# Optimization experiments

Measured on AMD Instinct MI355X. Metric: run time of the kernel, lower is better.

The kernel has to match this reference:

```python
import jax, jax.numpy as jnp
import numpy as np

D_MODEL = 1024
EXPAND = 4
D_INNER = EXPAND * D_MODEL  # 4096
D_STATE = 16
D_CONV = 4
DT_RANK = (D_MODEL + 15) // 16  # 64
B_SZ, L_SEQ = 2, 2048
EPS = 1e-5


def _quantize(w):
    # round(clamp(w / mean|w|, -1, 1)) -> ternary weights
    s = w / (jnp.mean(jnp.abs(w)) + 1e-8)
    return jnp.round(jnp.clip(s, -1.0, 1.0))


def setup_inputs() -> dict:
    key = jax.random.key(0)
    ks = jax.random.split(key, 16)
    f32 = jnp.float32
    x = jax.random.normal(ks[0], (B_SZ, L_SEQ, D_MODEL), dtype=f32)
    # LayerNorms
    g1 = jnp.ones((D_MODEL,), f32); b1 = jnp.zeros((D_MODEL,), f32)
    g2 = jnp.ones((D_MODEL,), f32); b2 = jnp.zeros((D_MODEL,), f32)
    # SwiGLU MLP (ternary-quantized weights, as in __init__)
    w1 = _quantize(jax.random.normal(ks[1], (EXPAND * D_MODEL, D_MODEL), f32) * 0.02)
    bias1 = jnp.zeros((EXPAND * D_MODEL,), f32)
    w2 = _quantize(jax.random.normal(ks[2], (D_MODEL, EXPAND * D_MODEL), f32) * 0.02)
    bias2 = jnp.zeros((D_MODEL,), f32)
    # Mamba params
    in_proj_w = jax.random.normal(ks[3], (2 * D_INNER, D_MODEL), f32) * 0.02
    conv_w = jax.random.normal(ks[4], (D_INNER, D_CONV), f32) * 0.2
    conv_b = jnp.zeros((D_INNER,), f32)
    x_proj_w = jax.random.normal(ks[5], (DT_RANK + 2 * D_STATE, D_INNER), f32) * 0.02
    dt_proj_w = jax.random.normal(ks[6], (D_INNER, DT_RANK), f32) * (DT_RANK ** -0.5)
    dt_proj_b = jnp.log(jnp.expm1(jnp.clip(
        jnp.exp(jax.random.uniform(ks[7], (D_INNER,), f32) * (np.log(0.1) - np.log(1e-3)) + np.log(1e-3)),
        1e-4, None)))  # standard mamba dt bias init
    A_log = jnp.log(jnp.broadcast_to(jnp.arange(1, D_STATE + 1, dtype=f32), (D_INNER, D_STATE)))
    D = jnp.ones((D_INNER,), f32)
    out_proj_w = jax.random.normal(ks[8], (D_MODEL, D_INNER), f32) * 0.02
    return dict(x=x, g1=g1, b1=b1, g2=g2, b2=b2, w1=w1, bias1=bias1, w2=w2, bias2=bias2,
                in_proj_w=in_proj_w, conv_w=conv_w, conv_b=conv_b, x_proj_w=x_proj_w,
                dt_proj_w=dt_proj_w, dt_proj_b=dt_proj_b, A_log=A_log, D=D,
                out_proj_w=out_proj_w)


def _layernorm(x, g, b):
    mu = jnp.mean(x, -1, keepdims=True)
    var = jnp.mean(jnp.square(x - mu), -1, keepdims=True)
    return (x - mu) * jax.lax.rsqrt(var + EPS) * g + b


def _mamba(xn, in_proj_w, conv_w, conv_b, x_proj_w, dt_proj_w, dt_proj_b, A_log, D, out_proj_w):
    B, L, _ = xn.shape
    xz = jnp.einsum('bld,ed->ble', xn, in_proj_w)  # [B,L,2*d_inner]
    u, z = jnp.split(xz, 2, axis=-1)
    # causal depthwise conv1d, kernel size D_CONV
    up = jnp.pad(u, ((0, 0), (D_CONV - 1, 0), (0, 0)))
    conv = conv_b + sum(up[:, k:k + L, :] * conv_w[:, k] for k in range(D_CONV))
    u = jax.nn.silu(conv)  # [B,L,d_inner]
    x_dbl = jnp.einsum('bld,ed->ble', u, x_proj_w)
    dt_in, Bm, Cm = jnp.split(x_dbl, [DT_RANK, DT_RANK + D_STATE], axis=-1)
    dt = jax.nn.softplus(jnp.einsum('blr,dr->bld', dt_in, dt_proj_w) + dt_proj_b)
    A = -jnp.exp(A_log)  # [d_inner, d_state]

    def step(h, inp):
        dt_t, B_t, C_t, u_t = inp  # [B,d_inner],[B,d_state],[B,d_state],[B,d_inner]
        dA = jnp.exp(dt_t[..., None] * A)              # [B,d_inner,d_state]
        h = dA * h + (dt_t * u_t)[..., None] * B_t[:, None, :]
        y = jnp.einsum('bds,bs->bd', h, C_t)
        return h, y

    h0 = jnp.zeros((B, D_INNER, D_STATE), xn.dtype)
    xs = (dt.swapaxes(0, 1), Bm.swapaxes(0, 1), Cm.swapaxes(0, 1), u.swapaxes(0, 1))
    _, ys = jax.lax.scan(step, h0, xs)
    y = ys.swapaxes(0, 1) + u * D
    y = y * jax.nn.silu(z)
    return jnp.einsum('ble,de->bld', y, out_proj_w)


def reference(x, g1, b1, g2, b2, w1, bias1, w2, bias2, in_proj_w, conv_w, conv_b,
              x_proj_w, dt_proj_w, dt_proj_b, A_log, D, out_proj_w):
    h = _layernorm(x, g1, b1)
    h = jax.nn.silu(jnp.einsum('bld,ed->ble', h, w1) + bias1)
    x = x + jnp.einsum('ble,de->bld', h, w2) + bias2
    x = x + _mamba(_layernorm(x, g2, b2), in_proj_w, conv_w, conv_b, x_proj_w,
                   dt_proj_w, dt_proj_b, A_log, D, out_proj_w)
    return x
```

## Files before the change

### kernel.cpp

```cpp
#include <hip/hip_runtime.h>
#include <cstdint>
#include <cstddef>


namespace {
constexpr int D_MODEL = 1024;
constexpr int D_INNER = 4096;
constexpr int D_STATE = 16;
constexpr int DT_RANK = 64;
constexpr int B_SZ    = 2;
constexpr int L_SEQ   = 2048;
constexpr int M_ROWS  = B_SZ * L_SEQ;
constexpr int LC      = 64;
constexpr int NCHUNK  = L_SEQ / LC;
}

typedef __bf16 bf16x8_t __attribute__((ext_vector_type(8)));
typedef float  f32x4    __attribute__((ext_vector_type(4)));

__device__ __forceinline__ unsigned short f2bf(float f) {
  union { float f; unsigned int u; } v; v.f = f;
  unsigned int r = (v.u + 0x7fffu + ((v.u >> 16) & 1u)) >> 16;
  return (unsigned short)r;
}
__device__ __forceinline__ float bf2f(unsigned short s) {
  union { unsigned int u; float f; } v; v.u = ((unsigned int)s) << 16;
  return v.f;
}

__device__ __forceinline__ float softplus_fast(float v) {
  const float e = __builtin_amdgcn_exp2f(-fabsf(v) * 1.44269504088896f);
  return fmaxf(v, 0.f) + 0.693147180559945f * __builtin_amdgcn_logf(1.f + e);
}

__device__ __forceinline__ void gload16(const void* g, void* l) {
  __builtin_amdgcn_global_load_lds(
      (const __attribute__((address_space(1))) unsigned int*)g,
      (__attribute__((address_space(3))) unsigned int*)l, 16, 0, 0);
}

__global__ __launch_bounds__(256)
void cvt6(const float* __restrict__ s0, unsigned short* __restrict__ d0,
          const float* __restrict__ s1, unsigned short* __restrict__ d1,
          const float* __restrict__ s2, unsigned short* __restrict__ d2,
          const float* __restrict__ s3, unsigned short* __restrict__ d3,
          const float* __restrict__ s4, unsigned short* __restrict__ d4,
          const float* __restrict__ s5, unsigned short* __restrict__ d5) {
  int blk = blockIdx.x;
  const float* s; unsigned short* d;
  if (blk < 4096)                  { s = s0; d = d0; }
  else if ((blk -= 4096) < 4096)   { s = s1; d = d1; }
  else if ((blk -= 4096) < 8192)   { s = s2; d = d2; }
  else if ((blk -= 8192) < 384)    { s = s3; d = d3; }
  else if ((blk -= 384) < 256)     { s = s4; d = d4; }
  else { blk -= 256;                 s = s5; d = d5; }
  const int i = blk * 1024 + threadIdx.x * 4;
  float4 v = *(const float4*)(s + i);
  ushort4 o; o.x = f2bf(v.x); o.y = f2bf(v.y); o.z = f2bf(v.z); o.w = f2bf(v.w);
  *(ushort4*)(d + i) = o;
}

__global__ __launch_bounds__(256) void ln_bf16(const float* __restrict__ x,
                                               const float* __restrict__ g,
                                               const float* __restrict__ b,
                                               unsigned short* __restrict__ out) {
  const int row = blockIdx.x;
  const int tid = threadIdx.x;
  const float4 v = *(const float4*)(x + (size_t)row * D_MODEL + tid * 4);
  float s  = v.x + v.y + v.z + v.w;
  float s2 = v.x*v.x + v.y*v.y + v.z*v.z + v.w*v.w;
#pragma unroll
  for (int o = 32; o >= 1; o >>= 1) { s += __shfl_xor(s, o); s2 += __shfl_xor(s2, o); }
  __shared__ float red[8];
  if ((tid & 63) == 0) { red[(tid >> 6) * 2] = s; red[(tid >> 6) * 2 + 1] = s2; }
  __syncthreads();
  s  = red[0] + red[2] + red[4] + red[6];
  s2 = red[1] + red[3] + red[5] + red[7];
  const float mu  = s * (1.f / D_MODEL);
  const float var = s2 * (1.f / D_MODEL) - mu * mu;
  const float rstd = rsqrtf(var + 1e-5f);
  const float4 gv = *(const float4*)(g + tid * 4);
  const float4 bv = *(const float4*)(b + tid * 4);
  ushort4 o;
  o.x = f2bf((v.x - mu) * rstd * gv.x + bv.x);
  o.y = f2bf((v.y - mu) * rstd * gv.y + bv.y);
  o.z = f2bf((v.z - mu) * rstd * gv.z + bv.z);
  o.w = f2bf((v.w - mu) * rstd * gv.w + bv.w);
  *(ushort4*)(out + (size_t)row * D_MODEL + tid * 4) = o;
}

__global__ __launch_bounds__(256)
void combine_ln(const float* __restrict__ part, const float* __restrict__ bias,
                const float* __restrict__ res, const float* __restrict__ g,
                const float* __restrict__ b, float* __restrict__ x2out,
                unsigned short* __restrict__ xnout) {
  const int row = blockIdx.x;
  const int tid = threadIdx.x;
  const size_t i4 = (size_t)row * D_MODEL + tid * 4;
  constexpr size_t S = (size_t)M_ROWS * D_MODEL;
  const float4 p0 = *(const float4*)(part + i4);
  const float4 p1 = *(const float4*)(part + S + i4);
  const float4 p2 = *(const float4*)(part + 2 * S + i4);
  const float4 p3 = *(const float4*)(part + 3 * S + i4);
  const float4 bv = *(const float4*)(bias + tid * 4);
  const float4 rv = *(const float4*)(res + i4);
  float4 v;
  v.x = p0.x + p1.x + p2.x + p3.x + bv.x + rv.x;
  v.y = p0.y + p1.y + p2.y + p3.y + bv.y + rv.y;
  v.z = p0.z + p1.z + p2.z + p3.z + bv.z + rv.z;
  v.w = p0.w + p1.w + p2.w + p3.w + bv.w + rv.w;
  *(float4*)(x2out + i4) = v;
  float s  = v.x + v.y + v.z + v.w;
  float s2 = v.x*v.x + v.y*v.y + v.z*v.z + v.w*v.w;
#pragma unroll
  for (int o = 32; o >= 1; o >>= 1) { s += __shfl_xor(s, o); s2 += __shfl_xor(s2, o); }
  __shared__ float red[8];
  if ((tid & 63) == 0) { red[(tid >> 6) * 2] = s; red[(tid >> 6) * 2 + 1] = s2; }
  __syncthreads();
  s  = red[0] + red[2] + red[4] + red[6];
  s2 = red[1] + red[3] + red[5] + red[7];
  const float mu  = s * (1.f / D_MODEL);
  const float var = s2 * (1.f / D_MODEL) - mu * mu;
  const float rstd = rsqrtf(var + 1e-5f);
  const float4 gv = *(const float4*)(g + tid * 4);
  const float4 b2 = *(const float4*)(b + tid * 4);
  ushort4 o;
  o.x = f2bf((v.x - mu) * rstd * gv.x + b2.x);
  o.y = f2bf((v.y - mu) * rstd * gv.y + b2.y);
  o.z = f2bf((v.z - mu) * rstd * gv.z + b2.z);
  o.w = f2bf((v.w - mu) * rstd * gv.w + b2.w);
  *(ushort4*)(xnout + i4) = o;
}

template<int EPI>
__global__ __launch_bounds__(512, 1)
void gemm256(const unsigned short* __restrict__ A, const unsigned short* __restrict__ W,
             int M, int N, int K, int lda, int ldw,
             const float* __restrict__ bias, void* __restrict__ out0) {
  __shared__ unsigned short As[2][256 * 64];
  __shared__ unsigned short Bs[2][256 * 64];
  const int tid  = threadIdx.x;
  const int w    = tid >> 6;
  const int lane = tid & 63;
  const int wr = w >> 2;
  const int wc = w & 3;
  const int fr = lane & 15;
  const int fq = lane >> 4;

  const int gx = gridDim.x, gy = gridDim.y;
  const int nwg = gx * gy;
  const int id  = blockIdx.y * gx + blockIdx.x;
  const int wid = (id & 7) * (nwg >> 3) + (id >> 3);
  const int n0 = (wid / gy) * 256;
  const int m0 = (wid % gy) * 256;

  const int srow  = tid >> 3;
  const int skelem = ((tid & 7) ^ (srow & 7)) * 8;

  int aslot[2];
#pragma unroll
  for (int ks = 0; ks < 2; ++ks) aslot[ks] = ((ks * 4 + fq) ^ (fr & 7)) * 8;

  f32x4 acc[8][4];
#pragma unroll
  for (int m = 0; m < 8; ++m)
#pragma unroll
    for (int n = 0; n < 4; ++n) acc[m][n] = f32x4{0.f, 0.f, 0.f, 0.f};

  const int NT = K >> 6;

  auto STAGE_HALF = [&](int half, int tn, unsigned short* Ad, unsigned short* Bd) {
    const int k0 = tn * 64;
    if (half < 2) {
#pragma unroll
      for (int li = 0; li < 2; ++li) {
        const int l = half * 2 + li;
        gload16(A + (size_t)(m0 + l * 64 + srow) * lda + k0 + skelem,
                Ad + (l * 64 + w * 8) * 64);
      }
    } else {
#pragma unroll
      for (int li = 0; li < 2; ++li) {
        const int l = (half - 2) * 2 + li;
        gload16(W + (size_t)(n0 + l * 64 + srow) * ldw + k0 + skelem,
                Bd + (l * 64 + w * 8) * 64);
      }
    }
  };

#pragma unroll
  for (int h = 0; h < 4; ++h) STAGE_HALF(h, 0, &As[0][0], &Bs[0][0]);
  asm volatile("s_waitcnt vmcnt(0)" ::: "memory");
  __builtin_amdgcn_sched_barrier(0);
  __builtin_amdgcn_s_barrier();
  __builtin_amdgcn_sched_barrier(0);

  for (int t = 0; t < NT; ++t) {
    const int cur = t & 1;
    const unsigned short* Ab = &As[cur][0];
    const unsigned short* Bb = &Bs[cur][0];
    unsigned short* Adn = &As[cur ^ 1][0];
    unsigned short* Bdn = &Bs[cur ^ 1][0];
    const bool more = (t + 1 < NT);

    bf16x8_t af[4][2], bflo[2][2], bfhi[2][2];

#pragma unroll
    for (int mfi = 0; mfi < 4; ++mfi)
#pragma unroll
      for (int ks = 0; ks < 2; ++ks)
        af[mfi][ks] = *(const bf16x8_t*)
            &Ab[(wr * 128 + mfi * 16 + fr) * 64 + aslot[ks]];
#pragma unroll
    for (int nfi = 0; nfi < 2; ++nfi)
#pragma unroll
      for (int ks = 0; ks < 2; ++ks)
        bflo[nfi][ks] = *(const bf16x8_t*)
            &Bb[(wc * 64 + nfi * 16 + fr) * 64 + aslot[ks]];
    if (more) { STAGE_HALF(0, t + 1, Adn, Bdn); STAGE_HALF(1, t + 1, Adn, Bdn); }
    asm volatile("s_waitcnt lgkmcnt(0)" ::: "memory");
    __builtin_amdgcn_sched_barrier(0);
    __builtin_amdgcn_s_barrier();
    __builtin_amdgcn_sched_barrier(0);
    __builtin_amdgcn_s_setprio(1);
#pragma unroll
    for (int mfi = 0; mfi < 4; ++mfi)
#pragma unroll
      for (int nfi = 0; nfi < 2; ++nfi)
#pragma unroll
        for (int ks = 0; ks < 2; ++ks)
          acc[mfi][nfi] = __builtin_amdgcn_mfma_f32_16x16x32_bf16(
              af[mfi][ks], bflo[nfi][ks], acc[mfi][nfi], 0, 0, 0);
    __builtin_amdgcn_s_setprio(0);
    __builtin_amdgcn_sched_barrier(0);

#pragma unroll
    for (int nfi = 0; nfi < 2; ++nfi)
#pragma unroll
      for (int ks = 0; ks < 2; ++ks)
        bfhi[nfi][ks] = *(const bf16x8_t*)
            &Bb[(wc * 64 + (2 + nfi) * 16 + fr) * 64 + aslot[ks]];
    if (more) { STAGE_HALF(2, t + 1, Adn, Bdn); STAGE_HALF(3, t + 1, Adn, Bdn); }
    asm volatile("s_waitcnt lgkmcnt(0)" ::: "memory");
    __builtin_amdgcn_sched_barrier(0);
    __builtin_amdgcn_s_barrier();
    __builtin_amdgcn_sched_barrier(0);
    __builtin_amdgcn_s_setprio(1);
#pragma unroll
    for (int mfi = 0; mfi < 4; ++mfi)
#pragma unroll
      for (int nfi = 0; nfi < 2; ++nfi)
#pragma unroll
        for (int ks = 0; ks < 2; ++ks)
          acc[mfi][2 + nfi] = __builtin_amdgcn_mfma_f32_16x16x32_bf16(
              af[mfi][ks], bfhi[nfi][ks], acc[mfi][2 + nfi], 0, 0, 0);
    __builtin_amdgcn_s_setprio(0);
    __builtin_amdgcn_sched_barrier(0);

#pragma unroll
    for (int mfi = 0; mfi < 4; ++mfi)
#pragma unroll
      for (int ks = 0; ks < 2; ++ks)
        af[mfi][ks] = *(const bf16x8_t*)
            &Ab[(wr * 128 + (4 + mfi) * 16 + fr) * 64 + aslot[ks]];
    asm volatile("s_waitcnt lgkmcnt(0)" ::: "memory");
    __builtin_amdgcn_sched_barrier(0);
    __builtin_amdgcn_s_barrier();
    __builtin_amdgcn_sched_barrier(0);
    __builtin_amdgcn_s_setprio(1);
#pragma unroll
    for (int mfi = 0; mfi < 4; ++mfi)
#pragma unroll
      for (int nfi = 0; nfi < 2; ++nfi)
#pragma unroll
        for (int ks = 0; ks < 2; ++ks)
          acc[4 + mfi][nfi] = __builtin_amdgcn_mfma_f32_16x16x32_bf16(
              af[mfi][ks], bflo[nfi][ks], acc[4 + mfi][nfi], 0, 0, 0);
    __builtin_amdgcn_s_setprio(0);
    __builtin_amdgcn_sched_barrier(0);

    __builtin_amdgcn_s_setprio(1);
#pragma unroll
    for (int mfi = 0; mfi < 4; ++mfi)
#pragma unroll
      for (int nfi = 0; nfi < 2; ++nfi)
#pragma unroll
        for (int ks = 0; ks < 2; ++ks)
          acc[4 + mfi][2 + nfi] = __builtin_amdgcn_mfma_f32_16x16x32_bf16(
              af[mfi][ks], bfhi[nfi][ks], acc[4 + mfi][2 + nfi], 0, 0, 0);
    __builtin_amdgcn_s_setprio(0);
    __builtin_amdgcn_sched_barrier(0);

    asm volatile("s_waitcnt vmcnt(0)" ::: "memory");
    __builtin_amdgcn_sched_barrier(0);
    __builtin_amdgcn_s_barrier();
    __builtin_amdgcn_sched_barrier(0);
  }

#pragma unroll
  for (int mf = 0; mf < 8; ++mf)
#pragma unroll
    for (int nf = 0; nf < 4; ++nf)
#pragma unroll
      for (int j = 0; j < 4; ++j) {
        const int r = m0 + wr * 128 + mf * 16 + fq * 4 + j;
        const int c = n0 + wc * 64 + nf * 16 + fr;
        float v = acc[mf][nf][j];
        if constexpr (EPI == 0) {
          v += bias[c];
          v = v / (1.f + __expf(-v));
          ((unsigned short*)out0)[(size_t)r * N + c] = f2bf(v);
        } else {
          ((unsigned short*)out0)[(size_t)r * N + c] = f2bf(v);
        }
      }
}

template<int EPI>
__global__ __launch_bounds__(256)
void gemm_bt(const unsigned short* __restrict__ A, const unsigned short* __restrict__ W,
             int M, int N, int K, int lda, int ldw, int ldc,
             const float* __restrict__ bias, const float* __restrict__ res,
             void* __restrict__ out0) {
  if constexpr (EPI == 6 || EPI == 8) {
    const size_t koff = (size_t)blockIdx.z * K;
    A += koff; W += koff;
    if constexpr (EPI == 6)
      out0 = (void*)((float*)out0 + (size_t)blockIdx.z * M * ldc);
    else
      out0 = (void*)((unsigned short*)out0 + (size_t)blockIdx.z * M * ldc);
  }
  const int gx = gridDim.x, gy = gridDim.y;
  const int nwg = gx * gy;
  const int id  = blockIdx.y * gx + blockIdx.x;
  const int wid = (id & 7) * (nwg >> 3) + (id >> 3);
  const int n0 = (wid / gy) * 128;
  const int m0 = (wid % gy) * 128;

  __shared__ unsigned short As[2][128 * 32];
  __shared__ unsigned short Bs[2][128 * 32];
  const int tid  = threadIdx.x;
  const int w    = tid >> 6;
  const int lane = tid & 63;
  const int wm = (w >> 1) * 64;
  const int wn = (w & 1) * 64;
  const int lrow = lane >> 2;
  const int lkb  = (lane & 3) * 8;
  const int fr   = lane & 15;
  const int fq   = lane >> 4;

  f32x4 acc[4][4];
#pragma unroll
  for (int m = 0; m < 4; ++m)
#pragma unroll
    for (int n = 0; n < 4; ++n) acc[m][n] = f32x4{0.f, 0.f, 0.f, 0.f};

  const int ar0 = m0 + (w * 2 + 0) * 16 + lrow;
  const int ar1 = m0 + (w * 2 + 1) * 16 + lrow;
  int br0 = n0 + (w * 2 + 0) * 16 + lrow; if (br0 > N - 1) br0 = N - 1;
  int br1 = n0 + (w * 2 + 1) * 16 + lrow; if (br1 > N - 1) br1 = N - 1;

  const int nk = K >> 5;
  auto STAGE = [&](int buf, int kt) {
    const int k0 = kt * 32;
    gload16(A + (size_t)ar0 * lda + k0 + lkb, &As[buf][(w * 2 + 0) * 512]);
    gload16(A + (size_t)ar1 * lda + k0 + lkb, &As[buf][(w * 2 + 1) * 512]);
    gload16(W + (size_t)br0 * ldw + k0 + lkb, &Bs[buf][(w * 2 + 0) * 512]);
    gload16(W + (size_t)br1 * ldw + k0 + lkb, &Bs[buf][(w * 2 + 1) * 512]);
  };
  STAGE(0, 0);
  if (nk > 1) STAGE(1, 1);

  for (int kt = 0; kt < nk; ++kt) {
    const int cur = kt & 1;
    if (kt + 1 < nk) asm volatile("s_waitcnt vmcnt(4)" ::: "memory");
    else             asm volatile("s_waitcnt vmcnt(0)" ::: "memory");
    __builtin_amdgcn_sched_barrier(0);
    __builtin_amdgcn_s_barrier();
    __builtin_amdgcn_sched_barrier(0);
    bf16x8_t af[4], bf[4];
#pragma unroll
    for (int m = 0; m < 4; ++m) af[m] = *(const bf16x8_t*)&As[cur][(wm + m * 16 + fr) * 32 + fq * 8];
#pragma unroll
    for (int n = 0; n < 4; ++n) bf[n] = *(const bf16x8_t*)&Bs[cur][(wn + n * 16 + fr) * 32 + fq * 8];
    __builtin_amdgcn_s_setprio(1);
#pragma unroll
    for (int m = 0; m < 4; ++m)
#pragma unroll
      for (int n = 0; n < 4; ++n)
        acc[m][n] = __builtin_amdgcn_mfma_f32_16x16x32_bf16(af[m], bf[n], acc[m][n], 0, 0, 0);
    __builtin_amdgcn_s_setprio(0);
    __builtin_amdgcn_sched_barrier(0);
    asm volatile("s_waitcnt lgkmcnt(0)" ::: "memory");
    __builtin_amdgcn_s_barrier();
    __builtin_amdgcn_sched_barrier(0);
    if (kt + 2 < nk) STAGE(cur, kt + 2);
  }

#pragma unroll
  for (int m = 0; m < 4; ++m)
#pragma unroll
    for (int n = 0; n < 4; ++n)
#pragma unroll
      for (int j = 0; j < 4; ++j) {
        const int r = m0 + wm + m * 16 + fq * 4 + j;
        const int c = n0 + wn + n * 16 + fr;
        if (c >= N) continue;
        float v = acc[m][n][j];
        if constexpr (EPI == 4) {
          v = softplus_fast(v + bias[c]);
          ((unsigned short*)out0)[(size_t)r * ldc + c] = f2bf(v);
        } else if constexpr (EPI == 6) {
          ((float*)out0)[(size_t)r * ldc + c] = v;
        } else {
          ((unsigned short*)out0)[(size_t)r * ldc + c] = f2bf(v);
        }
      }
}

__global__ __launch_bounds__(256)
void splitk_combine_bf(const unsigned short* __restrict__ part,
                       const float* __restrict__ res, float* __restrict__ out) {
  const size_t i4 = ((size_t)blockIdx.x * 256 + threadIdx.x) * 4;
  constexpr size_t S = (size_t)M_ROWS * D_MODEL;
  float a0 = 0.f, a1 = 0.f, a2 = 0.f, a3 = 0.f;
#pragma unroll
  for (int z = 0; z < 4; ++z) {
    const ushort4 p = *(const ushort4*)(part + z * S + i4);
    a0 += bf2f(p.x); a1 += bf2f(p.y); a2 += bf2f(p.z); a3 += bf2f(p.w);
  }
  const float4 r = *(const float4*)(res + i4);
  *(float4*)(out + i4) = float4{a0 + r.x, a1 + r.y, a2 + r.z, a3 + r.w};
}

__global__ __launch_bounds__(256)
void conv_silu_k(const unsigned short* __restrict__ xz, const float* __restrict__ cw,
                 const float* __restrict__ cb, unsigned short* __restrict__ uc) {
  const size_t idx = (size_t)blockIdx.x * 256 + threadIdx.x;
  const int d   = (int)(idx & (D_INNER - 1));
  const int row = (int)(idx >> 12);
  const int l   = row & (L_SEQ - 1);
  const float4 w4 = *(const float4*)(cw + d * 4);
  const unsigned short* up = xz + (size_t)row * (2 * D_INNER) + d;
  float acc = cb[d];
  if (l >= 3) acc += bf2f(up[-(ptrdiff_t)3 * 2 * D_INNER]) * w4.x;
  if (l >= 2) acc += bf2f(up[-(ptrdiff_t)2 * 2 * D_INNER]) * w4.y;
  if (l >= 1) acc += bf2f(up[-(ptrdiff_t)1 * 2 * D_INNER]) * w4.z;
  acc += bf2f(up[0]) * w4.w;
  const float r = acc / (1.f + __expf(-acc));
  uc[(size_t)row * D_INNER + d] = f2bf(r);
}

__global__ __launch_bounds__(256)
void xproj_combine(const float* __restrict__ part, unsigned short* __restrict__ dtin,
                   float* __restrict__ Bm, float* __restrict__ Cm) {
  const int idx = blockIdx.x * 256 + threadIdx.x;
  const int r = idx / 96, c = idx - r * 96;
  constexpr size_t S = (size_t)M_ROWS * 96;
  const float v = part[idx] + part[idx + S] + part[idx + 2 * S] + part[idx + 3 * S];
  if (c < DT_RANK)            dtin[(size_t)r * DT_RANK + c] = f2bf(v);
  else if (c < DT_RANK + 16)  Bm[(size_t)r * 16 + (c - DT_RANK)] = v;
  else                        Cm[(size_t)r * 16 + (c - DT_RANK - 16)] = v;
}

__global__ __launch_bounds__(128)
void scan_part(const unsigned short* __restrict__ dt, const unsigned short* __restrict__ uc,
               const float* __restrict__ Bm, const float* __restrict__ A_log,
               float* __restrict__ Q, float* __restrict__ sumdt) {
  __shared__ float sB[LC][D_STATE];
  const int lt = threadIdx.x;
  const int d  = blockIdx.x * 128 + lt;
  const int c  = blockIdx.y;
  const int b  = blockIdx.z;
  const size_t rowbase = (size_t)b * L_SEQ + (size_t)c * LC;
#pragma unroll
  for (int i = 0; i < 2; ++i)
    ((float4*)&sB[0][0])[lt + i * 128] =
        ((const float4*)(Bm + rowbase * D_STATE))[lt + i * 128];
  float Ap[D_STATE];
#pragma unroll
  for (int s = 0; s < D_STATE; ++s)
    Ap[s] = -__expf(A_log[d * D_STATE + s]) * 1.44269504088896f;
  float h[D_STATE];
#pragma unroll
  for (int s = 0; s < D_STATE; ++s) h[s] = 0.f;
  float sdt = 0.f;
  __syncthreads();
  for (int t = 0; t < LC; ++t) {
    const size_t row = rowbase + t;
    const float dtv = bf2f(dt[row * D_INNER + d]);
    const float uv  = bf2f(uc[row * D_INNER + d]);
    sdt += dtv;
    const float du = dtv * uv;
    const float4* bp = (const float4*)&sB[t][0];
    const float4 b0 = bp[0], b1 = bp[1], b2 = bp[2], b3 = bp[3];
    const float Bv[16] = {b0.x,b0.y,b0.z,b0.w, b1.x,b1.y,b1.z,b1.w,
                          b2.x,b2.y,b2.z,b2.w, b3.x,b3.y,b3.z,b3.w};
#pragma unroll
    for (int s = 0; s < D_STATE; ++s) {
      const float dA = __builtin_amdgcn_exp2f(dtv * Ap[s]);
      h[s] = fmaf(dA, h[s], du * Bv[s]);
    }
  }
  float* q = Q + ((((size_t)b * NCHUNK + c) * D_INNER + d) << 4);
#pragma unroll
  for (int s = 0; s < D_STATE; s += 4)
    *(float4*)(q + s) = float4{h[s], h[s+1], h[s+2], h[s+3]};
  sumdt[((size_t)b * NCHUNK + c) * D_INNER + d] = sdt;
}

__global__ __launch_bounds__(256)
void scan_carry(float* __restrict__ Q, const float* __restrict__ sumdt,
                const float* __restrict__ A_log) {
  const int idx = blockIdx.x * 256 + threadIdx.x;
  const int s = idx & 15;
  const int d = (idx >> 4) & (D_INNER - 1);
  const int b = idx >> 16;
  const float Ap = -__expf(A_log[d * D_STATE + s]) * 1.44269504088896f;
  float h = 0.f;
  for (int c = 0; c < NCHUNK; ++c) {
    const size_t base = ((size_t)b * NCHUNK + c) * D_INNER;
    const size_t qoff = ((base + d) << 4) + s;
    const float q = Q[qoff];
    const float P = __builtin_amdgcn_exp2f(sumdt[base + d] * Ap);
    Q[qoff] = h;
    h = fmaf(P, h, q);
  }
}

__global__ __launch_bounds__(128)
void scan_final(const unsigned short* __restrict__ dt, const unsigned short* __restrict__ uc,
                const float* __restrict__ Bm, const float* __restrict__ Cm,
                unsigned short* __restrict__ xz, const float* __restrict__ A_log,
                const float* __restrict__ Dvec, const float* __restrict__ Hin) {
  __shared__ float sB[LC][D_STATE];
  __shared__ float sC[LC][D_STATE];
  const int lt = threadIdx.x;
  const int d  = blockIdx.x * 128 + lt;
  const int c  = blockIdx.y;
  const int b  = blockIdx.z;
  const size_t rowbase = (size_t)b * L_SEQ + (size_t)c * LC;
#pragma unroll
  for (int i = 0; i < 2; ++i) {
    ((float4*)&sB[0][0])[lt + i * 128] =
        ((const float4*)(Bm + rowbase * D_STATE))[lt + i * 128];
    ((float4*)&sC[0][0])[lt + i * 128] =
        ((const float4*)(Cm + rowbase * D_STATE))[lt + i * 128];
  }
  float Ap[D_STATE];
#pragma unroll
  for (int s = 0; s < D_STATE; ++s)
    Ap[s] = -__expf(A_log[d * D_STATE + s]) * 1.44269504088896f;
  float h[D_STATE];
  const float* hin = Hin + ((((size_t)b * NCHUNK + c) * D_INNER + d) << 4);
#pragma unroll
  for (int s = 0; s < D_STATE; s += 4) {
    const float4 hv = *(const float4*)(hin + s);
    h[s] = hv.x; h[s+1] = hv.y; h[s+2] = hv.z; h[s+3] = hv.w;
  }
  const float Dv = Dvec[d];
  __syncthreads();
  for (int t = 0; t < LC; ++t) {
    const size_t row = rowbase + t;
    const float dtv = bf2f(dt[row * D_INNER + d]);
    const float uv  = bf2f(uc[row * D_INNER + d]);
    const float zv  = bf2f(xz[row * (2 * D_INNER) + D_INNER + d]);
    const float du = dtv * uv;
    const float4* bp = (const float4*)&sB[t][0];
    const float4 b0 = bp[0], b1 = bp[1], b2 = bp[2], b3 = bp[3];
    const float Bv[16] = {b0.x,b0.y,b0.z,b0.w, b1.x,b1.y,b1.z,b1.w,
                          b2.x,b2.y,b2.z,b2.w, b3.x,b3.y,b3.z,b3.w};
    const float4* cp = (const float4*)&sC[t][0];
    const float4 c0 = cp[0], c1 = cp[1], c2 = cp[2], c3 = cp[3];
    const float Cv[16] = {c0.x,c0.y,c0.z,c0.w, c1.x,c1.y,c1.z,c1.w,
                          c2.x,c2.y,c2.z,c2.w, c3.x,c3.y,c3.z,c3.w};
    float y0 = 0.f, y1 = 0.f;
#pragma unroll
    for (int s = 0; s < D_STATE; s += 2) {
      const float dA0 = __builtin_amdgcn_exp2f(dtv * Ap[s]);
      const float dA1 = __builtin_amdgcn_exp2f(dtv * Ap[s+1]);
      h[s]   = fmaf(dA0, h[s],   du * Bv[s]);
      h[s+1] = fmaf(dA1, h[s+1], du * Bv[s+1]);
      y0 = fmaf(h[s],   Cv[s],   y0);
      y1 = fmaf(h[s+1], Cv[s+1], y1);
    }
    const float yo = (y0 + y1 + uv * Dv) * (zv / (1.f + __expf(-zv)));
    xz[row * (2 * D_INNER) + d] = f2bf(yo);
  }
}

extern "C" void kernel_launch(void* const* d_in, const int* in_sizes, int n_in,
                              void* d_out, int out_size, void* d_ws, size_t ws_size,
                              hipStream_t stream) {
  (void)in_sizes; (void)n_in; (void)out_size; (void)ws_size;
  const float* x     = (const float*)d_in[0];
  const float* g1    = (const float*)d_in[1];
  const float* b1    = (const float*)d_in[2];
  const float* g2    = (const float*)d_in[3];
  const float* b2    = (const float*)d_in[4];
  const float* w1    = (const float*)d_in[5];
  const float* bias1 = (const float*)d_in[6];
  const float* w2    = (const float*)d_in[7];
  const float* bias2 = (const float*)d_in[8];
  const float* ipw   = (const float*)d_in[9];
  const float* cw    = (const float*)d_in[10];
  const float* cb    = (const float*)d_in[11];
  const float* xpw   = (const float*)d_in[12];
  const float* dtw   = (const float*)d_in[13];
  const float* dtbv  = (const float*)d_in[14];
  const float* A_log = (const float*)d_in[15];
  const float* Dvec  = (const float*)d_in[16];
  const float* opw   = (const float*)d_in[17];

  char* ws = (char*)d_ws;
  size_t off = 0;
  auto alloc = [&](size_t bytes) { void* p = ws + off; off = (off + bytes + 255) & ~(size_t)255; return p; };

  unsigned short* w1b  = (unsigned short*)alloc((size_t)D_INNER * D_MODEL * 2);
  unsigned short* w2b  = (unsigned short*)alloc((size_t)D_MODEL * D_INNER * 2);
  unsigned short* ipb  = (unsigned short*)alloc((size_t)2 * D_INNER * D_MODEL * 2);
  unsigned short* xpb  = (unsigned short*)alloc((size_t)96 * D_INNER * 2);
  unsigned short* dtb  = (unsigned short*)alloc((size_t)D_INNER * DT_RANK * 2);
  unsigned short* opb  = (unsigned short*)alloc((size_t)D_MODEL * D_INNER * 2);
  unsigned short* xn   = (unsigned short*)alloc((size_t)M_ROWS * D_MODEL * 2);
  unsigned short* hid  = (unsigned short*)alloc((size_t)M_ROWS * D_INNER * 2);
  float*          x2   = (float*)alloc((size_t)M_ROWS * D_MODEL * 4);
  unsigned short* xz   = (unsigned short*)alloc((size_t)M_ROWS * 2 * D_INNER * 2);
  unsigned short* dtbf = (unsigned short*)alloc((size_t)M_ROWS * D_INNER * 2);
  unsigned short* dtin = (unsigned short*)alloc((size_t)M_ROWS * DT_RANK * 2);
  float*          Bmb  = (float*)alloc((size_t)M_ROWS * 16 * 4);
  float*          Cmb  = (float*)alloc((size_t)M_ROWS * 16 * 4);
  float*          xpart= (float*)alloc((size_t)4 * M_ROWS * 96 * 4);
  float*          Qbuf = (float*)alloc((size_t)B_SZ * NCHUNK * D_INNER * 16 * 4);
  unsigned short* ucb  = hid;
  float*          sumdt = xpart;
  float*          pA   = (float*)xz;
  unsigned short* pB   = dtbf;

  cvt6<<<21120, 256, 0, stream>>>(w1, w1b, w2, w2b, ipw, ipb, xpw, xpb, dtw, dtb, opw, opb);

  ln_bf16<<<M_ROWS, 256, 0, stream>>>(x, g1, b1, xn);
  gemm256<0><<<dim3(D_INNER / 256, M_ROWS / 256), 512, 0, stream>>>(
      xn, w1b, M_ROWS, D_INNER, D_MODEL, D_MODEL, D_MODEL, bias1, hid);
  gemm_bt<6><<<dim3(D_MODEL / 128, M_ROWS / 128, 4), 256, 0, stream>>>(
      hid, w2b, M_ROWS, D_MODEL, D_INNER / 4, D_INNER, D_INNER, D_MODEL, nullptr, nullptr, pA);
  combine_ln<<<M_ROWS, 256, 0, stream>>>(pA, bias2, x, g2, b2, x2, xn);

  gemm256<2><<<dim3(2 * D_INNER / 256, M_ROWS / 256), 512, 0, stream>>>(
      xn, ipb, M_ROWS, 2 * D_INNER, D_MODEL, D_MODEL, D_MODEL, nullptr, xz);
  conv_silu_k<<<(size_t)M_ROWS * D_INNER / 256, 256, 0, stream>>>(xz, cw, cb, ucb);

  gemm_bt<6><<<dim3(1, M_ROWS / 128, 4), 256, 0, stream>>>(
      ucb, xpb, M_ROWS, 96, 1024, D_INNER, D_INNER, 96,
      nullptr, nullptr, xpart);
  xproj_combine<<<M_ROWS * 96 / 256, 256, 0, stream>>>(xpart, dtin, Bmb, Cmb);

  gemm_bt<4><<<dim3(D_INNER / 128, M_ROWS / 128), 256, 0, stream>>>(
      dtin, dtb, M_ROWS, D_INNER, DT_RANK, DT_RANK, DT_RANK, D_INNER, dtbv, nullptr, dtbf);

  scan_part<<<dim3(D_INNER / 128, NCHUNK, B_SZ), 128, 0, stream>>>(
      dtbf, ucb, Bmb, A_log, Qbuf, sumdt);
  scan_carry<<<B_SZ * D_INNER * 16 / 256, 256, 0, stream>>>(Qbuf, sumdt, A_log);
  scan_final<<<dim3(D_INNER / 128, NCHUNK, B_SZ), 128, 0, stream>>>(
      dtbf, ucb, Bmb, Cmb, xz, A_log, Dvec, Qbuf);

  gemm_bt<8><<<dim3(D_MODEL / 128, M_ROWS / 128, 4), 256, 0, stream>>>(
      xz, opb, M_ROWS, D_MODEL, D_INNER / 4, 2 * D_INNER, D_INNER, D_MODEL,
      nullptr, nullptr, pB);
  splitk_combine_bf<<<M_ROWS * D_MODEL / 1024, 256, 0, stream>>>(pB, x2, (float*)d_out);
}
```

Baseline: 521.6 us.

## Store W2 split-K partials in bf16, vectorize conv, split x_proj K further

The W2 split-K GEMM now writes bf16 partials instead of fp32, and combine_ln sums them in fp32, halving partial-buffer traffic. The depthwise conv+SiLU kernel now handles 8 channels per thread with 16-byte vector loads and stores. The x_proj GEMM is split 8 ways over K instead of 4 to raise its block count, with a guard added to the block-id swizzle for small grids. Rounding partials to bf16 adds precision loss to the residual path.

```diff
diff --git a/kernel.cpp b/kernel.cpp
--- a/kernel.cpp
+++ b/kernel.cpp
@@ -17,6 +17,7 @@
 
 typedef __bf16 bf16x8_t __attribute__((ext_vector_type(8)));
 typedef float  f32x4    __attribute__((ext_vector_type(4)));
+typedef unsigned short us8 __attribute__((ext_vector_type(8)));
 
 __device__ __forceinline__ unsigned short f2bf(float f) {
   union { float f; unsigned int u; } v; v.f = f;
@@ -90,7 +91,7 @@
 }
 
 __global__ __launch_bounds__(256)
-void combine_ln(const float* __restrict__ part, const float* __restrict__ bias,
+void combine_ln(const unsigned short* __restrict__ part, const float* __restrict__ bias,
                 const float* __restrict__ res, const float* __restrict__ g,
                 const float* __restrict__ b, float* __restrict__ x2out,
                 unsigned short* __restrict__ xnout) {
@@ -98,17 +99,19 @@
   const int tid = threadIdx.x;
   const size_t i4 = (size_t)row * D_MODEL + tid * 4;
   constexpr size_t S = (size_t)M_ROWS * D_MODEL;
-  const float4 p0 = *(const float4*)(part + i4);
-  const float4 p1 = *(const float4*)(part + S + i4);
-  const float4 p2 = *(const float4*)(part + 2 * S + i4);
-  const float4 p3 = *(const float4*)(part + 3 * S + i4);
+  float a0 = 0.f, a1 = 0.f, a2 = 0.f, a3 = 0.f;
+#pragma unroll
+  for (int z = 0; z < 4; ++z) {
+    const ushort4 p = *(const ushort4*)(part + z * S + i4);
+    a0 += bf2f(p.x); a1 += bf2f(p.y); a2 += bf2f(p.z); a3 += bf2f(p.w);
+  }
   const float4 bv = *(const float4*)(bias + tid * 4);
   const float4 rv = *(const float4*)(res + i4);
   float4 v;
-  v.x = p0.x + p1.x + p2.x + p3.x + bv.x + rv.x;
-  v.y = p0.y + p1.y + p2.y + p3.y + bv.y + rv.y;
-  v.z = p0.z + p1.z + p2.z + p3.z + bv.z + rv.z;
-  v.w = p0.w + p1.w + p2.w + p3.w + bv.w + rv.w;
+  v.x = a0 + bv.x + rv.x;
+  v.y = a1 + bv.y + rv.y;
+  v.z = a2 + bv.z + rv.z;
+  v.w = a3 + bv.w + rv.w;
   *(float4*)(x2out + i4) = v;
   float s  = v.x + v.y + v.z + v.w;
   float s2 = v.x*v.x + v.y*v.y + v.z*v.z + v.w*v.w;
@@ -333,7 +336,7 @@
   const int gx = gridDim.x, gy = gridDim.y;
   const int nwg = gx * gy;
   const int id  = blockIdx.y * gx + blockIdx.x;
-  const int wid = (id & 7) * (nwg >> 3) + (id >> 3);
+  const int wid = (nwg >= 8) ? ((id & 7) * (nwg >> 3) + (id >> 3)) : id;
   const int n0 = (wid / gy) * 128;
   const int m0 = (wid % gy) * 128;
 
@@ -437,18 +440,27 @@
 void conv_silu_k(const unsigned short* __restrict__ xz, const float* __restrict__ cw,
                  const float* __restrict__ cb, unsigned short* __restrict__ uc) {
   const size_t idx = (size_t)blockIdx.x * 256 + threadIdx.x;
-  const int d   = (int)(idx & (D_INNER - 1));
-  const int row = (int)(idx >> 12);
+  const int dg  = (int)(idx & 511) * 8;
+  const int row = (int)(idx >> 9);
   const int l   = row & (L_SEQ - 1);
-  const float4 w4 = *(const float4*)(cw + d * 4);
-  const unsigned short* up = xz + (size_t)row * (2 * D_INNER) + d;
-  float acc = cb[d];
-  if (l >= 3) acc += bf2f(up[-(ptrdiff_t)3 * 2 * D_INNER]) * w4.x;
-  if (l >= 2) acc += bf2f(up[-(ptrdiff_t)2 * 2 * D_INNER]) * w4.y;
-  if (l >= 1) acc += bf2f(up[-(ptrdiff_t)1 * 2 * D_INNER]) * w4.z;
-  acc += bf2f(up[0]) * w4.w;
-  const float r = acc / (1.f + __expf(-acc));
-  uc[(size_t)row * D_INNER + d] = f2bf(r);
+  const unsigned short* up = xz + (size_t)row * (2 * D_INNER) + dg;
+  us8 t0 = {0,0,0,0,0,0,0,0}, t1 = {0,0,0,0,0,0,0,0}, t2 = {0,0,0,0,0,0,0,0};
+  const us8 t3 = *(const us8*)(up);
+  if (l >= 1) t2 = *(const us8*)(up - (ptrdiff_t)1 * 2 * D_INNER);
+  if (l >= 2) t1 = *(const us8*)(up - (ptrdiff_t)2 * 2 * D_INNER);
+  if (l >= 3) t0 = *(const us8*)(up - (ptrdiff_t)3 * 2 * D_INNER);
+  us8 o;
+#pragma unroll
+  for (int j = 0; j < 8; ++j) {
+    const float4 w4 = *(const float4*)(cw + (dg + j) * 4);
+    float acc = cb[dg + j];
+    acc += bf2f(t0[j]) * w4.x;
+    acc += bf2f(t1[j]) * w4.y;
+    acc += bf2f(t2[j]) * w4.z;
+    acc += bf2f(t3[j]) * w4.w;
+    o[j] = f2bf(acc / (1.f + __expf(-acc)));
+  }
+  *(us8*)(uc + (size_t)row * D_INNER + dg) = o;
 }
 
 __global__ __launch_bounds__(256)
@@ -457,7 +469,9 @@
   const int idx = blockIdx.x * 256 + threadIdx.x;
   const int r = idx / 96, c = idx - r * 96;
   constexpr size_t S = (size_t)M_ROWS * 96;
-  const float v = part[idx] + part[idx + S] + part[idx + 2 * S] + part[idx + 3 * S];
+  float v = 0.f;
+#pragma unroll
+  for (int z = 0; z < 8; ++z) v += part[idx + z * S];
   if (c < DT_RANK)            dtin[(size_t)r * DT_RANK + c] = f2bf(v);
   else if (c < DT_RANK + 16)  Bm[(size_t)r * 16 + (c - DT_RANK)] = v;
   else                        Cm[(size_t)r * 16 + (c - DT_RANK - 16)] = v;
@@ -630,11 +644,11 @@
   unsigned short* dtin = (unsigned short*)alloc((size_t)M_ROWS * DT_RANK * 2);
   float*          Bmb  = (float*)alloc((size_t)M_ROWS * 16 * 4);
   float*          Cmb  = (float*)alloc((size_t)M_ROWS * 16 * 4);
-  float*          xpart= (float*)alloc((size_t)4 * M_ROWS * 96 * 4);
+  float*          xpart= (float*)alloc((size_t)8 * M_ROWS * 96 * 4);
   float*          Qbuf = (float*)alloc((size_t)B_SZ * NCHUNK * D_INNER * 16 * 4);
   unsigned short* ucb  = hid;
   float*          sumdt = xpart;
-  float*          pA   = (float*)xz;
+  unsigned short* pA   = (unsigned short*)xz;
   unsigned short* pB   = dtbf;
 
   cvt6<<<21120, 256, 0, stream>>>(w1, w1b, w2, w2b, ipw, ipb, xpw, xpb, dtw, dtb, opw, opb);
@@ -642,16 +656,16 @@
   ln_bf16<<<M_ROWS, 256, 0, stream>>>(x, g1, b1, xn);
   gemm256<0><<<dim3(D_INNER / 256, M_ROWS / 256), 512, 0, stream>>>(
       xn, w1b, M_ROWS, D_INNER, D_MODEL, D_MODEL, D_MODEL, bias1, hid);
-  gemm_bt<6><<<dim3(D_MODEL / 128, M_ROWS / 128, 4), 256, 0, stream>>>(
+  gemm_bt<8><<<dim3(D_MODEL / 128, M_ROWS / 128, 4), 256, 0, stream>>>(
       hid, w2b, M_ROWS, D_MODEL, D_INNER / 4, D_INNER, D_INNER, D_MODEL, nullptr, nullptr, pA);
   combine_ln<<<M_ROWS, 256, 0, stream>>>(pA, bias2, x, g2, b2, x2, xn);
 
   gemm256<2><<<dim3(2 * D_INNER / 256, M_ROWS / 256), 512, 0, stream>>>(
       xn, ipb, M_ROWS, 2 * D_INNER, D_MODEL, D_MODEL, D_MODEL, nullptr, xz);
-  conv_silu_k<<<(size_t)M_ROWS * D_INNER / 256, 256, 0, stream>>>(xz, cw, cb, ucb);
-
-  gemm_bt<6><<<dim3(1, M_ROWS / 128, 4), 256, 0, stream>>>(
-      ucb, xpb, M_ROWS, 96, 1024, D_INNER, D_INNER, 96,
+  conv_silu_k<<<(size_t)M_ROWS * 512 / 256, 256, 0, stream>>>(xz, cw, cb, ucb);
+
+  gemm_bt<6><<<dim3(1, M_ROWS / 128, 8), 256, 0, stream>>>(
+      ucb, xpb, M_ROWS, 96, 512, D_INNER, D_INNER, 96,
       nullptr, nullptr, xpart);
   xproj_combine<<<M_ROWS * 96 / 256, 256, 0, stream>>>(xpart, dtin, Bmb, Cmb);
 
```

After: 510.0 us. -2.2%, faster.
